# Kernel tuning notes

Measured on AMD Instinct MI355X. Metric: run time of the kernel, lower is better.

Reference implementation:

```python
import jax, jax.numpy as jnp
import numpy as np

B, N, C, H = 128, 8732, 512, 19  # batch, priors, channels, feature map side
IMG = 300.0
FG = 19


def setup_inputs() -> dict:
    key = jax.random.key(0)
    ks = jax.random.split(key, 10)
    loc = jax.random.normal(ks[0], (B, N, 4), jnp.float32) * 0.5
    conf = jax.random.normal(ks[1], (B, N, 2), jnp.float32)
    priors = jax.random.uniform(ks[2], (N, 4), jnp.float32, minval=0.05, maxval=0.95)
    features = jax.random.normal(ks[3], (B, C, H, H), jnp.float32)
    w1 = jax.random.normal(ks[4], (C, 4096), jnp.float32) * 0.01
    b1 = jnp.zeros((4096,), jnp.float32)
    w2 = jax.random.normal(ks[5], (4096, 4096), jnp.float32) * 0.01
    b2 = jnp.zeros((4096,), jnp.float32)
    w3 = jax.random.normal(ks[6], (4096, FG), jnp.float32) * 0.01
    b3 = jnp.zeros((FG,), jnp.float32)
    return {"loc": loc, "conf": conf, "priors": priors, "features": features,
            "w1": w1, "b1": b1, "w2": w2, "b2": b2, "w3": w3, "b3": b3}


def _decode(loc, priors):
    # SSD decode, variances=[0.1, 0.2]; priors are (cx, cy, w, h)
    cxcy = priors[:, :2] + loc[..., :2] * 0.1 * priors[:, 2:]
    wh = priors[:, 2:] * jnp.exp(loc[..., 2:] * 0.2)
    xy1 = cxcy - 0.5 * wh
    return jnp.concatenate([xy1, xy1 + wh], axis=-1)  # [B,N,4] corner form


def _best_prior(loc, conf, priors):
    boxes = _decode(loc, priors)                       # [B,N,4]
    probs = jax.nn.softmax(conf, axis=-1)              # [B,N,2]
    car = jnp.argmax(probs, axis=-1) == 1              # [B,N] argmax class == car
    score = jnp.where(car, probs[..., 1], -jnp.inf)
    best = jnp.argmax(score, axis=-1)                  # [B]
    best_box = jnp.take_along_axis(boxes, best[:, None, None], axis=1)[:, 0]  # [B,4]
    has_car = jnp.any(car, axis=-1)                    # [B]
    geom = (best_box[:, 2] > best_box[:, 0]) & (best_box[:, 3] > best_box[:, 1])
    valid = has_car & geom
    result = jnp.where(has_car[:, None], best_box, 0.0)
    result = jnp.clip(result, 0.0, 1.0)
    return result, valid


def _extract(features, boxes, valid):
    # per-box crop + global max pool -> [B,C], zero for invalid boxes
    ceil_num = features.shape[2]
    step = IMG / ceil_num
    b = jnp.clip(boxes * IMG, 0.0, IMG) / step
    b = jnp.floor(jnp.clip(b, 0.0, ceil_num - 1.0)).astype(jnp.int32)  # [B,4]=x1,y1,x2,y2
    r = jnp.arange(ceil_num)
    mh = (r[None, :] >= b[:, 1:2]) & (r[None, :] <= b[:, 3:4])  # [B,H] rows
    mw = (r[None, :] >= b[:, 0:1]) & (r[None, :] <= b[:, 2:3])  # [B,W] cols
    mask = mh[:, None, :, None] & mw[:, None, None, :]          # [B,1,H,W]
    m = jnp.max(jnp.where(mask, features, -jnp.inf), axis=(2, 3))  # [B,C]
    return jnp.where(valid[:, None], m, 0.0)


def reference(loc, conf, priors, features, w1, b1, w2, b2, w3, b3):
    boxes, valid = _best_prior(loc, conf, priors)
    feat = _extract(features, boxes, valid)             # [B,512]
    h = jax.nn.relu(feat @ w1 + b1)
    h = jax.nn.relu(h @ w2 + b2)
    fg_cls = h @ w3 + b3                                # [B,19]
    return fg_cls, boxes, valid.astype(jnp.int32)
```

## Files before the change

### kernel.cpp

```cpp
#include <hip/hip_runtime.h>
#include <hip/hip_bf16.h>
#include <math.h>

#define BATCH 128
#define NPRI  8732
#define CCH   512
#define HH    19
#define NHID  4096
#define FGC   19

typedef unsigned short u16;
typedef __attribute__((ext_vector_type(8))) short bf16x8;
typedef __attribute__((ext_vector_type(4))) float f32x4;

__device__ __forceinline__ u16 f2bf(float f) {
  unsigned u = __float_as_uint(f);
  u += 0x7fff + ((u >> 16) & 1);
  return (u16)(u >> 16);
}

__global__ void k_best(const float* __restrict__ conf,
                       const float* __restrict__ loc,
                       const float* __restrict__ priors,
                       float* __restrict__ out_boxes,
                       float* __restrict__ out_valid,
                       int4* __restrict__ crop, int* __restrict__ vflag) {
  int b = blockIdx.x;
  int t = threadIdx.x;
  const float4* cb = (const float4*)(conf + (size_t)b * NPRI * 2);
  float bd = -INFINITY; int bn = 0x7fffffff;
  for (int j = t; j < NPRI / 2; j += 256) {
    float4 v = cb[j];
    float d0 = v.y - v.x, d1 = v.w - v.z;
    if (d0 > bd) { bd = d0; bn = 2 * j; }
    if (d1 > bd) { bd = d1; bn = 2 * j + 1; }
  }
  __shared__ float ls[256]; __shared__ int li[256];
  ls[t] = bd; li[t] = bn;
  __syncthreads();
  for (int off = 128; off > 0; off >>= 1) {
    if (t < off) {
      float s2 = ls[t + off]; int n2 = li[t + off];
      if (s2 > ls[t] || (s2 == ls[t] && n2 < li[t])) { ls[t] = s2; li[t] = n2; }
    }
    __syncthreads();
  }
  if (t == 0) {
    float bdf = ls[0]; int bnf = li[0];
    bool hc = bdf > 0.0f;
    float r0 = 0.f, r1 = 0.f, r2 = 0.f, r3 = 0.f;
    bool valid = false;
    if (hc) {
      const float* lp = loc + ((size_t)b * NPRI + bnf) * 4;
      const float* pp = priors + (size_t)bnf * 4;
      float l0 = lp[0], l1 = lp[1], l2 = lp[2], l3 = lp[3];
      float pcx = pp[0], pcy = pp[1], pw = pp[2], ph = pp[3];
      float cx = pcx + (l0 * 0.1f) * pw;
      float cy = pcy + (l1 * 0.1f) * ph;
      float w = pw * expf(l2 * 0.2f);
      float h = ph * expf(l3 * 0.2f);
      float x1 = cx - 0.5f * w, y1 = cy - 0.5f * h;
      float x2 = x1 + w, y2 = y1 + h;
      valid = (x2 > x1) && (y2 > y1);
      r0 = fminf(fmaxf(x1, 0.f), 1.f);
      r1 = fminf(fmaxf(y1, 0.f), 1.f);
      r2 = fminf(fmaxf(x2, 0.f), 1.f);
      r3 = fminf(fmaxf(y2, 0.f), 1.f);
    }
    out_boxes[b * 4 + 0] = r0; out_boxes[b * 4 + 1] = r1;
    out_boxes[b * 4 + 2] = r2; out_boxes[b * 4 + 3] = r3;
    out_valid[b] = valid ? 1.0f : 0.0f;
    const float stepF = (float)(300.0 / 19.0);
    float q0 = fminf(fmaxf(r0 * 300.0f, 0.0f), 300.0f) / stepF;
    float q1 = fminf(fmaxf(r1 * 300.0f, 0.0f), 300.0f) / stepF;
    float q2 = fminf(fmaxf(r2 * 300.0f, 0.0f), 300.0f) / stepF;
    float q3 = fminf(fmaxf(r3 * 300.0f, 0.0f), 300.0f) / stepF;
    int ix1 = (int)floorf(fminf(fmaxf(q0, 0.0f), 18.0f));
    int iy1 = (int)floorf(fminf(fmaxf(q1, 0.0f), 18.0f));
    int ix2 = (int)floorf(fminf(fmaxf(q2, 0.0f), 18.0f));
    int iy2 = (int)floorf(fminf(fmaxf(q3, 0.0f), 18.0f));
    crop[b] = make_int4(ix1, iy1, ix2, iy2);
    vflag[b] = valid ? 1 : 0;
  }
}

__global__ void k_extract(const float* __restrict__ fin,
                          const int4* __restrict__ crop,
                          const int* __restrict__ vflag,
                          u16* __restrict__ feat) {
  int blk = blockIdx.x;
  int b = blk >> 7;
  int tile = blk & 127;
  int wave = threadIdx.x >> 6;
  int lane = threadIdx.x & 63;
  int c = tile * 4 + wave;
  if (!vflag[b]) {
    if (lane == 0) feat[b * CCH + c] = 0;
    return;
  }
  int4 cr = crop[b];
  int wcnt = cr.z - cr.x + 1;
  int cnt = wcnt * (cr.w - cr.y + 1);
  const float* p = fin + (size_t)(b * CCH + c) * (HH * HH);
  float m = -INFINITY;
  for (int i = lane; i < cnt; i += 64) {
    int yy = cr.y + i / wcnt;
    int xx = cr.x + i % wcnt;
    m = fmaxf(m, p[yy * HH + xx]);
  }
  #pragma unroll
  for (int off = 32; off > 0; off >>= 1) m = fmaxf(m, __shfl_xor(m, off));
  if (lane == 0) feat[b * CCH + c] = f2bf(m);
}

template <int KSPL>
__global__ __launch_bounds__(256) void k_mfma(const u16* __restrict__ A,
                                              const float* __restrict__ W,
                                              float* __restrict__ part, int K) {
  const int N = NHID;
  int nb = blockIdx.x;
  int ks = blockIdx.y;
  int Kper = K / KSPL;
  int k0b = ks * Kper;
  int t = threadIdx.x;
  int lane = t & 63, wave = t >> 6;
  int q = lane >> 4, r = lane & 15;

  __shared__ u16 As[128 * 40];
  __shared__ u16 Bs[64 * 40];

  int wm = (wave & 1) * 64;
  int wn = (wave >> 1) * 32;
  int n0 = nb * 64;

  f32x4 acc[4][2];
  #pragma unroll
  for (int i = 0; i < 4; i++)
    #pragma unroll
    for (int j = 0; j < 2; j++) {
      acc[i][j].x = 0.f; acc[i][j].y = 0.f; acc[i][j].z = 0.f; acc[i][j].w = 0.f;
    }

  int am = t >> 1, ah = (t & 1) * 16;
  int kp = t >> 4;
  int n4 = (t & 15) * 4;

  for (int k0 = k0b; k0 < k0b + Kper; k0 += 32) {
    const u16* asrc = A + (size_t)am * K + k0 + ah;
    uint4 a0 = *(const uint4*)asrc;
    uint4 a1 = *(const uint4*)(asrc + 8);
    const float* wsrc = W + (size_t)(k0 + 2 * kp) * N + n0 + n4;
    float4 w0 = *(const float4*)wsrc;
    float4 w1v = *(const float4*)(wsrc + N);
    __syncthreads();
    *(uint4*)&As[am * 40 + ah]     = a0;
    *(uint4*)&As[am * 40 + ah + 8] = a1;
    {
      __hip_bfloat162 p0 = __float22bfloat162_rn(make_float2(w0.x, w1v.x));
      __hip_bfloat162 p1 = __float22bfloat162_rn(make_float2(w0.y, w1v.y));
      __hip_bfloat162 p2 = __float22bfloat162_rn(make_float2(w0.z, w1v.z));
      __hip_bfloat162 p3 = __float22bfloat162_rn(make_float2(w0.w, w1v.w));
      *(__hip_bfloat162*)&Bs[(n4 + 0) * 40 + 2 * kp] = p0;
      *(__hip_bfloat162*)&Bs[(n4 + 1) * 40 + 2 * kp] = p1;
      *(__hip_bfloat162*)&Bs[(n4 + 2) * 40 + 2 * kp] = p2;
      *(__hip_bfloat162*)&Bs[(n4 + 3) * 40 + 2 * kp] = p3;
    }
    __syncthreads();
    bf16x8 af[4], bfr[2];
    #pragma unroll
    for (int i = 0; i < 4; i++)
      af[i] = *(const bf16x8*)&As[(wm + 16 * i + r) * 40 + q * 8];
    #pragma unroll
    for (int j = 0; j < 2; j++)
      bfr[j] = *(const bf16x8*)&Bs[(wn + 16 * j + r) * 40 + q * 8];
    #pragma unroll
    for (int i = 0; i < 4; i++)
      #pragma unroll
      for (int j = 0; j < 2; j++)
        acc[i][j] = __builtin_amdgcn_mfma_f32_16x16x32_bf16(af[i], bfr[j],
                                                            acc[i][j], 0, 0, 0);
  }

  float* dst = part + (size_t)ks * (BATCH * NHID);
  #pragma unroll
  for (int i = 0; i < 4; i++)
    #pragma unroll
    for (int j = 0; j < 2; j++) {
      int col = n0 + wn + 16 * j + r;
      #pragma unroll
      for (int reg = 0; reg < 4; reg++) {
        int row = wm + 16 * i + q * 4 + reg;
        dst[(size_t)row * N + col] = acc[i][j][reg];
      }
    }
}

template <int KSPL>
__global__ void k_finalize_bf16(const float* __restrict__ part,
                                const float* __restrict__ bias,
                                u16* __restrict__ outb) {
  int idx = (blockIdx.x * 256 + threadIdx.x) * 4;
  float4 s = *(const float4*)(part + idx);
  #pragma unroll
  for (int p = 1; p < KSPL; p++) {
    float4 v = *(const float4*)(part + (size_t)p * (BATCH * NHID) + idx);
    s.x += v.x; s.y += v.y; s.z += v.z; s.w += v.w;
  }
  float4 bv = *(const float4*)(bias + (idx & (NHID - 1)));
  s.x = fmaxf(s.x + bv.x, 0.0f); s.y = fmaxf(s.y + bv.y, 0.0f);
  s.z = fmaxf(s.z + bv.z, 0.0f); s.w = fmaxf(s.w + bv.w, 0.0f);
  ushort4 o;
  o.x = f2bf(s.x); o.y = f2bf(s.y); o.z = f2bf(s.z); o.w = f2bf(s.w);
  *(ushort4*)(outb + idx) = o;
}

__global__ void k_gemm3p(const float* __restrict__ part,
                         const float* __restrict__ b2,
                         const float* __restrict__ w3,
                         float* __restrict__ part3) {
  int kc = blockIdx.x;
  int t = threadIdx.x;
  __shared__ float wl[32 * FGC];
  __shared__ float ht[128 * 33];
  for (int i = t; i < 32 * FGC; i += 128) wl[i] = w3[kc * 32 * FGC + i];
  int klane = t & 31, mg = t >> 5;
  float bv = b2[kc * 32 + klane];
  for (int i = 0; i < 32; i++) {
    int m = mg * 32 + i;
    const float* pp = part + (size_t)m * NHID + kc * 32 + klane;
    float s = pp[0];
    #pragma unroll
    for (int p = 1; p < 8; p++) s += pp[(size_t)p * (BATCH * NHID)];
    ht[m * 33 + klane] = fmaxf(s + bv, 0.0f);
  }
  __syncthreads();
  float acc[FGC];
  #pragma unroll
  for (int j = 0; j < FGC; j++) acc[j] = 0.0f;
  const float* hp = &ht[t * 33];
  for (int k = 0; k < 32; k++) {
    float hv = hp[k];
    const float* wp = &wl[k * FGC];
    #pragma unroll
    for (int j = 0; j < FGC; j++) acc[j] += hv * wp[j];
  }
  float* dst = part3 + (size_t)kc * (BATCH * FGC) + t * FGC;
  #pragma unroll
  for (int j = 0; j < FGC; j++) dst[j] = acc[j];
}

__global__ void k_fin3(const float* __restrict__ part3,
                       const float* __restrict__ b3,
                       float* __restrict__ out) {
  int j = blockIdx.x * 256 + threadIdx.x;
  if (j >= BATCH * FGC) return;
  float s = 0.0f;
  for (int p = 0; p < 128; p++) s += part3[(size_t)p * (BATCH * FGC) + j];
  out[j] = s + b3[j % FGC];
}

extern "C" void kernel_launch(void* const* d_in, const int* in_sizes, int n_in,
                              void* d_out, int out_size, void* d_ws, size_t ws_size,
                              hipStream_t stream) {
  const float* loc      = (const float*)d_in[0];
  const float* conf     = (const float*)d_in[1];
  const float* priors   = (const float*)d_in[2];
  const float* features = (const float*)d_in[3];
  const float* w1 = (const float*)d_in[4];
  const float* b1 = (const float*)d_in[5];
  const float* w2 = (const float*)d_in[6];
  const float* b2 = (const float*)d_in[7];
  const float* w3 = (const float*)d_in[8];
  const float* b3 = (const float*)d_in[9];
  float* out = (float*)d_out;

  char* ws = (char*)d_ws;
  float* part  = (float*)ws;
  float* part3 = (float*)(ws + (size_t)16 * 1024 * 1024);
  u16*   featb = (u16*)(ws + (size_t)20 * 1024 * 1024);
  u16*   h1b   = (u16*)(ws + (size_t)20 * 1024 * 1024 + 256 * 1024);
  int4*  crop  = (int4*)(ws + (size_t)21 * 1024 * 1024 + 512 * 1024);
  int*   vfl   = (int*)(crop + BATCH);

  k_best<<<BATCH, 256, 0, stream>>>(conf, loc, priors,
                                    out + BATCH * FGC,
                                    out + BATCH * FGC + BATCH * 4, crop, vfl);
  k_extract<<<BATCH * (CCH / 4), 256, 0, stream>>>(features, crop, vfl, featb);
  k_mfma<4><<<dim3(64, 4), 256, 0, stream>>>(featb, w1, part, CCH);
  k_finalize_bf16<4><<<512, 256, 0, stream>>>(part, b1, h1b);
  k_mfma<8><<<dim3(64, 8), 256, 0, stream>>>(h1b, w2, part, NHID);
  k_gemm3p<<<128, 128, 0, stream>>>(part, b2, w3, part3);
  k_fin3<<<10, 256, 0, stream>>>(part3, b3, out);
}
```

Baseline: 261.1 us.

## Templatize MFMA K-tile with swizzled LDS, fuse final GEMM3 reduction

The MFMA GEMM kernel is templated on the K tile size. The large W2 GEMM now uses a 64-wide K tile, which halves barrier round trips per K step and issues more loads per iteration, and an XOR swizzle on the B tile in LDS reduces bank conflicts. The third layer replaces the two-kernel partial-sum scheme with one block per batch row. Each block reduces the split-K partials, applies bias and ReLU, multiplies by W3 and reduces across waves. This drops a launch and the part3 round trip, but every block now reads all of W3 from global memory.

```diff
diff --git a/kernel.cpp b/kernel.cpp
--- a/kernel.cpp
+++ b/kernel.cpp
@@ -1,5 +1,4 @@
 #include <hip/hip_runtime.h>
-#include <hip/hip_bf16.h>
 #include <math.h>
 
 #define BATCH 128
@@ -113,11 +112,13 @@
   if (lane == 0) feat[b * CCH + c] = f2bf(m);
 }
 
-template <int KSPL>
+template <int BK, int KSPL>
 __global__ __launch_bounds__(256) void k_mfma(const u16* __restrict__ A,
                                               const float* __restrict__ W,
                                               float* __restrict__ part, int K) {
   const int N = NHID;
+  const int STR = BK + 8;
+  const int GM = BK / 8 - 1;
   int nb = blockIdx.x;
   int ks = blockIdx.y;
   int Kper = K / KSPL;
@@ -126,8 +127,8 @@
   int lane = t & 63, wave = t >> 6;
   int q = lane >> 4, r = lane & 15;
 
-  __shared__ u16 As[128 * 40];
-  __shared__ u16 Bs[64 * 40];
+  __shared__ u16 As[128 * STR];
+  __shared__ u16 Bs[64 * STR];
 
   int wm = (wave & 1) * 64;
   int wn = (wave >> 1) * 32;
@@ -141,44 +142,60 @@
       acc[i][j].x = 0.f; acc[i][j].y = 0.f; acc[i][j].z = 0.f; acc[i][j].w = 0.f;
     }
 
-  int am = t >> 1, ah = (t & 1) * 16;
+  int am = t >> 1, ah = (t & 1) * (BK / 2);
   int kp = t >> 4;
   int n4 = (t & 15) * 4;
 
-  for (int k0 = k0b; k0 < k0b + Kper; k0 += 32) {
-    const u16* asrc = A + (size_t)am * K + k0 + ah;
-    uint4 a0 = *(const uint4*)asrc;
-    uint4 a1 = *(const uint4*)(asrc + 8);
-    const float* wsrc = W + (size_t)(k0 + 2 * kp) * N + n0 + n4;
-    float4 w0 = *(const float4*)wsrc;
-    float4 w1v = *(const float4*)(wsrc + N);
+  for (int k0 = k0b; k0 < k0b + Kper; k0 += BK) {
+    uint4 areg[BK / 16];
+    #pragma unroll
+    for (int u = 0; u < BK / 16; u++)
+      areg[u] = *(const uint4*)(A + (size_t)am * K + k0 + ah + 8 * u);
+    float4 wr0[BK / 32], wr1[BK / 32];
+    #pragma unroll
+    for (int c = 0; c < BK / 32; c++) {
+      int kpp = kp + 16 * c;
+      const float* wsrc = W + (size_t)(k0 + 2 * kpp) * N + n0 + n4;
+      wr0[c] = *(const float4*)wsrc;
+      wr1[c] = *(const float4*)(wsrc + N);
+    }
     __syncthreads();
-    *(uint4*)&As[am * 40 + ah]     = a0;
-    *(uint4*)&As[am * 40 + ah + 8] = a1;
-    {
-      __hip_bfloat162 p0 = __float22bfloat162_rn(make_float2(w0.x, w1v.x));
-      __hip_bfloat162 p1 = __float22bfloat162_rn(make_float2(w0.y, w1v.y));
-      __hip_bfloat162 p2 = __float22bfloat162_rn(make_float2(w0.z, w1v.z));
-      __hip_bfloat162 p3 = __float22bfloat162_rn(make_float2(w0.w, w1v.w));
-      *(__hip_bfloat162*)&Bs[(n4 + 0) * 40 + 2 * kp] = p0;
-      *(__hip_bfloat162*)&Bs[(n4 + 1) * 40 + 2 * kp] = p1;
-      *(__hip_bfloat162*)&Bs[(n4 + 2) * 40 + 2 * kp] = p2;
-      *(__hip_bfloat162*)&Bs[(n4 + 3) * 40 + 2 * kp] = p3;
+    #pragma unroll
+    for (int u = 0; u < BK / 16; u++)
+      *(uint4*)&As[am * STR + ah + 8 * u] = areg[u];
+    #pragma unroll
+    for (int c = 0; c < BK / 32; c++) {
+      int kpp = kp + 16 * c;
+      int g = kpp >> 2, kl = 2 * (kpp & 3);
+      float f0[4] = {wr0[c].x, wr0[c].y, wr0[c].z, wr0[c].w};
+      float f1[4] = {wr1[c].x, wr1[c].y, wr1[c].z, wr1[c].w};
+      #pragma unroll
+      for (int j = 0; j < 4; j++) {
+        int row = n4 + j;
+        int e = row * STR + ((g ^ ((row >> 3) & GM)) * 8) + kl;
+        *(unsigned*)&Bs[e] = (unsigned)f2bf(f0[j]) | ((unsigned)f2bf(f1[j]) << 16);
+      }
     }
     __syncthreads();
-    bf16x8 af[4], bfr[2];
-    #pragma unroll
-    for (int i = 0; i < 4; i++)
-      af[i] = *(const bf16x8*)&As[(wm + 16 * i + r) * 40 + q * 8];
-    #pragma unroll
-    for (int j = 0; j < 2; j++)
-      bfr[j] = *(const bf16x8*)&Bs[(wn + 16 * j + r) * 40 + q * 8];
-    #pragma unroll
-    for (int i = 0; i < 4; i++)
-      #pragma unroll
-      for (int j = 0; j < 2; j++)
-        acc[i][j] = __builtin_amdgcn_mfma_f32_16x16x32_bf16(af[i], bfr[j],
-                                                            acc[i][j], 0, 0, 0);
+    #pragma unroll
+    for (int kk = 0; kk < BK / 32; kk++) {
+      bf16x8 af[4], bfr[2];
+      #pragma unroll
+      for (int i = 0; i < 4; i++)
+        af[i] = *(const bf16x8*)&As[(wm + 16 * i + r) * STR + kk * 32 + q * 8];
+      #pragma unroll
+      for (int j = 0; j < 2; j++) {
+        int row = wn + 16 * j + r;
+        int gq = q + 4 * kk;
+        bfr[j] = *(const bf16x8*)&Bs[row * STR + ((gq ^ ((row >> 3) & GM)) * 8)];
+      }
+      #pragma unroll
+      for (int i = 0; i < 4; i++)
+        #pragma unroll
+        for (int j = 0; j < 2; j++)
+          acc[i][j] = __builtin_amdgcn_mfma_f32_16x16x32_bf16(af[i], bfr[j],
+                                                              acc[i][j], 0, 0, 0);
+    }
   }
 
   float* dst = part + (size_t)ks * (BATCH * NHID);
@@ -214,49 +231,55 @@
   *(ushort4*)(outb + idx) = o;
 }
 
-__global__ void k_gemm3p(const float* __restrict__ part,
-                         const float* __restrict__ b2,
-                         const float* __restrict__ w3,
-                         float* __restrict__ part3) {
-  int kc = blockIdx.x;
+__global__ __launch_bounds__(256) void k_gemm3(const float* __restrict__ part,
+                                               const float* __restrict__ b2,
+                                               const float* __restrict__ w3,
+                                               const float* __restrict__ b3,
+                                               float* __restrict__ out) {
+  int b = blockIdx.x;
   int t = threadIdx.x;
-  __shared__ float wl[32 * FGC];
-  __shared__ float ht[128 * 33];
-  for (int i = t; i < 32 * FGC; i += 128) wl[i] = w3[kc * 32 * FGC + i];
-  int klane = t & 31, mg = t >> 5;
-  float bv = b2[kc * 32 + klane];
-  for (int i = 0; i < 32; i++) {
-    int m = mg * 32 + i;
-    const float* pp = part + (size_t)m * NHID + kc * 32 + klane;
-    float s = pp[0];
-    #pragma unroll
-    for (int p = 1; p < 8; p++) s += pp[(size_t)p * (BATCH * NHID)];
-    ht[m * 33 + klane] = fmaxf(s + bv, 0.0f);
+  __shared__ float hrow[NHID];
+  __shared__ float xred[4 * FGC];
+  #pragma unroll
+  for (int c = 0; c < 4; c++) {
+    int idx = c * 1024 + t * 4;
+    const float* pp = part + (size_t)b * NHID + idx;
+    float4 s = *(const float4*)pp;
+    #pragma unroll
+    for (int p = 1; p < 8; p++) {
+      float4 v = *(const float4*)(pp + (size_t)p * (BATCH * NHID));
+      s.x += v.x; s.y += v.y; s.z += v.z; s.w += v.w;
+    }
+    float4 bv = *(const float4*)(b2 + idx);
+    s.x = fmaxf(s.x + bv.x, 0.0f); s.y = fmaxf(s.y + bv.y, 0.0f);
+    s.z = fmaxf(s.z + bv.z, 0.0f); s.w = fmaxf(s.w + bv.w, 0.0f);
+    *(float4*)&hrow[idx] = s;
   }
   __syncthreads();
   float acc[FGC];
   #pragma unroll
   for (int j = 0; j < FGC; j++) acc[j] = 0.0f;
-  const float* hp = &ht[t * 33];
-  for (int k = 0; k < 32; k++) {
-    float hv = hp[k];
-    const float* wp = &wl[k * FGC];
+  for (int c = 0; c < 16; c++) {
+    int k = c * 256 + t;
+    float hv = hrow[k];
+    const float* wp = w3 + (size_t)k * FGC;
     #pragma unroll
     for (int j = 0; j < FGC; j++) acc[j] += hv * wp[j];
   }
-  float* dst = part3 + (size_t)kc * (BATCH * FGC) + t * FGC;
-  #pragma unroll
-  for (int j = 0; j < FGC; j++) dst[j] = acc[j];
-}
-
-__global__ void k_fin3(const float* __restrict__ part3,
-                       const float* __restrict__ b3,
-                       float* __restrict__ out) {
-  int j = blockIdx.x * 256 + threadIdx.x;
-  if (j >= BATCH * FGC) return;
-  float s = 0.0f;
-  for (int p = 0; p < 128; p++) s += part3[(size_t)p * (BATCH * FGC) + j];
-  out[j] = s + b3[j % FGC];
+  #pragma unroll
+  for (int j = 0; j < FGC; j++)
+    #pragma unroll
+    for (int off = 32; off > 0; off >>= 1)
+      acc[j] += __shfl_xor(acc[j], off);
+  int lane = t & 63, wv = t >> 6;
+  if (lane == 0) {
+    #pragma unroll
+    for (int j = 0; j < FGC; j++) xred[wv * FGC + j] = acc[j];
+  }
+  __syncthreads();
+  if (t < FGC)
+    out[b * FGC + t] = xred[t] + xred[FGC + t] + xred[2 * FGC + t] +
+                       xred[3 * FGC + t] + b3[t];
 }
 
 extern "C" void kernel_launch(void* const* d_in, const int* in_sizes, int n_in,
@@ -276,19 +299,17 @@
 
   char* ws = (char*)d_ws;
   float* part  = (float*)ws;
-  float* part3 = (float*)(ws + (size_t)16 * 1024 * 1024);
-  u16*   featb = (u16*)(ws + (size_t)20 * 1024 * 1024);
-  u16*   h1b   = (u16*)(ws + (size_t)20 * 1024 * 1024 + 256 * 1024);
-  int4*  crop  = (int4*)(ws + (size_t)21 * 1024 * 1024 + 512 * 1024);
+  u16*   featb = (u16*)(ws + (size_t)16 * 1024 * 1024);
+  u16*   h1b   = (u16*)(ws + (size_t)16 * 1024 * 1024 + 256 * 1024);
+  int4*  crop  = (int4*)(ws + (size_t)18 * 1024 * 1024);
   int*   vfl   = (int*)(crop + BATCH);
 
   k_best<<<BATCH, 256, 0, stream>>>(conf, loc, priors,
                                     out + BATCH * FGC,
                                     out + BATCH * FGC + BATCH * 4, crop, vfl);
   k_extract<<<BATCH * (CCH / 4), 256, 0, stream>>>(features, crop, vfl, featb);
-  k_mfma<4><<<dim3(64, 4), 256, 0, stream>>>(featb, w1, part, CCH);
+  k_mfma<32, 4><<<dim3(64, 4), 256, 0, stream>>>(featb, w1, part, CCH);
   k_finalize_bf16<4><<<512, 256, 0, stream>>>(part, b1, h1b);
-  k_mfma<8><<<dim3(64, 8), 256, 0, stream>>>(h1b, w2, part, NHID);
-  k_gemm3p<<<128, 128, 0, stream>>>(part, b2, w3, part3);
-  k_fin3<<<10, 256, 0, stream>>>(part3, b3, out);
-}
+  k_mfma<64, 8><<<dim3(64, 8), 256, 0, stream>>>(h1b, w2, part, NHID);
+  k_gemm3<<<BATCH, 256, 0, stream>>>(part, b2, w3, b3, out);
+}
```

After: 265.0 us. About the same (+1.5%).
